# Kernel optimization log

Hardware: AMD Instinct MI355X
Metric: run time of the kernel (lower is better)

The kernel has to match this reference:

```python
import jax, jax.numpy as jnp
import numpy as np

B, T_ENC, T_DEC = 16, 256, 200
N_MELS, ENC_DIM, PRENET, ARNN, DRNN, ATT, NF, KS = 80, 512, 256, 1024, 1024, 128, 32, 31


def _init(k, shape, fan_in):
    return jax.random.normal(k, shape, dtype=jnp.float32) / np.sqrt(fan_in).astype(np.float32)


def setup_inputs() -> dict:
    ks = jax.random.split(jax.random.key(0), 20)
    return {
        "memory": jax.random.normal(ks[0], (B, T_ENC, ENC_DIM), jnp.float32),
        "decoder_inputs": jax.random.normal(ks[1], (B, N_MELS, T_DEC), jnp.float32),
        "memory_lengths": jax.random.randint(ks[2], (B,), T_ENC // 2, T_ENC + 1),
        "prenet_W1": _init(ks[3], (N_MELS, PRENET), N_MELS),
        "prenet_W2": _init(ks[4], (PRENET, PRENET), PRENET),
        "arnn_Wih": _init(ks[5], (PRENET + ENC_DIM, 4 * ARNN), PRENET + ENC_DIM),
        "arnn_Whh": _init(ks[6], (ARNN, 4 * ARNN), ARNN),
        "arnn_b": jnp.zeros((4 * ARNN,), jnp.float32),
        "Wq": _init(ks[7], (ARNN, ATT), ARNN),
        "Wmem": _init(ks[8], (ENC_DIM, ATT), ENC_DIM),
        "v_w": _init(ks[9], (ATT,), ATT),
        "loc_conv_W": _init(ks[10], (NF, 2, KS), 2 * KS),
        "loc_dense_W": _init(ks[11], (NF, ATT), NF),
        "drnn_Wih": _init(ks[12], (ARNN + ENC_DIM, 4 * DRNN), ARNN + ENC_DIM),
        "drnn_Whh": _init(ks[13], (DRNN, 4 * DRNN), DRNN),
        "drnn_b": jnp.zeros((4 * DRNN,), jnp.float32),
        "proj_W": _init(ks[14], (DRNN + ENC_DIM, N_MELS), DRNN + ENC_DIM),
        "proj_b": jnp.zeros((N_MELS,), jnp.float32),
        "gate_W": _init(ks[15], (DRNN + ENC_DIM, 1), DRNN + ENC_DIM),
        "gate_b": jnp.zeros((1,), jnp.float32),
    }


def _lstm_cell(x, h, c, Wih, Whh, b):
    z = x @ Wih + h @ Whh + b  # [B, 4H], torch gate order i,f,g,o
    i, f, g, o = jnp.split(z, 4, axis=-1)
    c_new = jax.nn.sigmoid(f) * c + jax.nn.sigmoid(i) * jnp.tanh(g)
    h_new = jax.nn.sigmoid(o) * jnp.tanh(c_new)
    return h_new, c_new


def reference(memory, decoder_inputs, memory_lengths, prenet_W1, prenet_W2,
              arnn_Wih, arnn_Whh, arnn_b, Wq, Wmem, v_w, loc_conv_W, loc_dense_W,
              drnn_Wih, drnn_Whh, drnn_b, proj_W, proj_b, gate_W, gate_b):
    dt = memory.dtype
    # parse_decoder_inputs + go-frame: [T_DEC+1, B, n_mels]
    di = jnp.transpose(decoder_inputs, (2, 0, 1))
    di = jnp.concatenate([jnp.zeros((1, B, N_MELS), dt), di], axis=0)
    # prenet (dropout hardcoded training=True in source; deterministic key here)
    k1, k2 = jax.random.split(jax.random.key(42))
    x = jax.nn.relu(di @ prenet_W1)
    x = x * jax.random.bernoulli(k1, 0.5, x.shape).astype(dt) * 2.0
    x = jax.nn.relu(x @ prenet_W2)
    x = x * jax.random.bernoulli(k2, 0.5, x.shape).astype(dt) * 2.0
    pre = x[:-1]  # [T_DEC, B, PRENET] (loop consumes first T_DEC frames)

    pm = memory @ Wmem  # processed_memory [B, T_enc, ATT]
    pad_mask = jnp.arange(T_ENC)[None, :] >= memory_lengths[:, None]  # [B, T_enc]
    pad = KS // 2

    def step(carry, xt):
        ah, ac, dh, dc, aw, awc, ctx = carry
        ah, ac = _lstm_cell(jnp.concatenate([xt, ctx], -1), ah, ac, arnn_Wih, arnn_Whh, arnn_b)
        # location-sensitive attention
        awcat = jnp.stack([aw, awc], axis=1)  # [B, 2, T_enc]
        loc = jax.lax.conv_general_dilated(awcat, loc_conv_W, (1,), [(pad, pad)],
                                           dimension_numbers=("NCH", "OIH", "NCH"))  # [B, NF, T_enc]
        loc = jnp.swapaxes(loc, 1, 2) @ loc_dense_W  # [B, T_enc, ATT]
        pq = ah @ Wq  # [B, ATT]
        e = jnp.tanh(pq[:, None, :] + loc + pm) @ v_w  # [B, T_enc]
        e = jnp.where(pad_mask, jnp.asarray(-1e9, dt), e)
        w = jax.nn.softmax(e, axis=1)
        ctx = jnp.einsum("bt,bte->be", w, memory)
        awc = awc + w
        dh, dc = _lstm_cell(jnp.concatenate([ah, ctx], -1), dh, dc, drnn_Wih, drnn_Whh, drnn_b)
        dhc = jnp.concatenate([dh, ctx], axis=1)
        mel = dhc @ proj_W + proj_b  # [B, n_mels]
        gate = (dhc @ gate_W + gate_b)[:, 0]  # [B]
        return (ah, ac, dh, dc, w, awc, ctx), (mel, gate, w)

    carry0 = (jnp.zeros((B, ARNN), dt), jnp.zeros((B, ARNN), dt),
              jnp.zeros((B, DRNN), dt), jnp.zeros((B, DRNN), dt),
              jnp.zeros((B, T_ENC), dt), jnp.zeros((B, T_ENC), dt),
              jnp.zeros((B, ENC_DIM), dt))
    _, (mels, gates, aligns) = jax.lax.scan(step, carry0, pre)
    mel_out = jnp.transpose(mels, (1, 2, 0))    # [B, n_mels, T_DEC]
    gate_out = jnp.transpose(gates, (1, 0))     # [B, T_DEC]
    align_out = jnp.transpose(aligns, (1, 0, 2))  # [B, T_DEC, T_enc]
    return mel_out, gate_out, align_out
```

## Files before the change

kernel.cpp:

```cpp
#include <hip/hip_runtime.h>
#include <stdint.h>

typedef unsigned short u16;
typedef _Float16 h2f16 __attribute__((ext_vector_type(2)));

#define BB    16
#define TENC  256
#define TDEC  200
#define NMELS 80
#define EDIM  512
#define PREN  256
#define ARN   1024
#define ATTN  128
#define NFILT 32
#define KSIZE 31

#define NBLK  256
#define NTHR  1024

#define OFF_AW     0
#define OFF_AWC    4096
#define OFF_AC     8192
#define OFF_DC     24576
#define OFF_XCAT1  40960
#define OFF_XCAT2  77824
#define STATE_F    118784
#define OFF_PRETU  118784
#define OFF_PMU    528384
#define OFF_Z1     790528
#define OFF_Z2     1249280
#define OFF_PQP    1773568
#define OFF_EBUF   1806336
#define OFF_BAR    1810432

__host__ __device__ inline void tf2x32(uint32_t k0, uint32_t k1, uint32_t x0, uint32_t x1,
                                       uint32_t &y0, uint32_t &y1) {
  uint32_t ks2 = k0 ^ k1 ^ 0x1BD11BDAu;
  x0 += k0; x1 += k1;
  const int R0[4] = {13, 15, 26, 6};
  const int R1[4] = {17, 29, 16, 24};
#pragma unroll
  for (int g = 0; g < 5; ++g) {
    const int *R = (g & 1) ? R1 : R0;
#pragma unroll
    for (int i = 0; i < 4; ++i) {
      x0 += x1;
      x1 = (x1 << R[i]) | (x1 >> (32 - R[i]));
      x1 ^= x0;
    }
    switch (g) {
      case 0: x0 += k1;  x1 += ks2 + 1u; break;
      case 1: x0 += ks2; x1 += k0 + 2u;  break;
      case 2: x0 += k0;  x1 += k1 + 3u;  break;
      case 3: x0 += k1;  x1 += ks2 + 4u; break;
      case 4: x0 += ks2; x1 += k0 + 5u;  break;
    }
  }
  y0 = x0; y1 = x1;
}

__device__ inline bool keep_mask(uint32_t k0, uint32_t k1, uint32_t idx) {
  uint32_t y0, y1;
  tf2x32(k0, k1, 0u, idx, y0, y1);
  return (((y0 ^ y1) >> 31) == 0u);
}

__device__ inline float bf2f(u16 v) {
  union { uint32_t u; float f; } x;
  x.u = ((uint32_t)v) << 16;
  return x.f;
}
__device__ inline u16 f2bf(float f) {
  union { float f; uint32_t u; } x;
  x.f = f;
  uint32_t r = ((x.u >> 16) & 1u) + 0x7FFFu;
  return (u16)((x.u + r) >> 16);
}
__device__ inline float sigm(float x) { return 1.f / (1.f + __expf(-x)); }
__device__ inline float ftanh(float x) {
  x = fminf(fmaxf(x, -15.f), 15.f);
  float e = __expf(2.f * x);
  return (e - 1.f) / (e + 1.f);
}

__device__ inline uint32_t packh2(float a, float b) {
  h2f16 h; h[0] = (_Float16)a; h[1] = (_Float16)b;
  union { h2f16 h; uint32_t u; } x; x.h = h; return x.u;
}
__device__ inline h2f16 u2h2(uint32_t u) {
  union { uint32_t u; h2f16 h; } x; x.u = u; return x.h;
}
__device__ inline float fdot2(h2f16 a, h2f16 b, float c) {
#if __has_builtin(__builtin_amdgcn_fdot2)
  return __builtin_amdgcn_fdot2(a, b, c, false);
#else
  return (float)a[0] * (float)b[0] + (float)a[1] * (float)b[1] + c;
#endif
}

__device__ inline float cload(const float *p) {
  uint32_t u = __hip_atomic_load((const uint32_t *)p, __ATOMIC_RELAXED,
                                 __HIP_MEMORY_SCOPE_AGENT);
  union { uint32_t u; float f; } x; x.u = u; return x.f;
}
__device__ inline void cstore(float *p, float v) {
  union { float f; uint32_t u; } x; x.f = v;
  __hip_atomic_store((uint32_t *)p, x.u, __ATOMIC_RELAXED,
                     __HIP_MEMORY_SCOPE_AGENT);
}
__device__ inline void cload8(const float *p, float &a, float &b) {
  unsigned long long u = __hip_atomic_load((const unsigned long long *)p,
                                           __ATOMIC_RELAXED,
                                           __HIP_MEMORY_SCOPE_AGENT);
  union { unsigned long long u; float f[2]; } x; x.u = u;
  a = x.f[0]; b = x.f[1];
}

__device__ inline void gsync(unsigned int *bar, unsigned int e, int cb) {
  __syncthreads();
  if (threadIdx.x == 0) {
    asm volatile("s_waitcnt vmcnt(0)" ::: "memory");
    int g = cb & 7;
    unsigned int *arr = bar + g * 64;
    unsigned int *gct = bar + 512;
    unsigned int *rel = bar + 576 + g * 64;
    unsigned int old = __hip_atomic_fetch_add(arr, 1u, __ATOMIC_RELAXED,
                                              __HIP_MEMORY_SCOPE_AGENT);
    if (old == e * 32u - 1u) {
      unsigned int o2 = __hip_atomic_fetch_add(gct, 1u, __ATOMIC_RELAXED,
                                               __HIP_MEMORY_SCOPE_AGENT);
      if (o2 == e * 8u - 1u) {
#pragma unroll
        for (int g2 = 0; g2 < 8; ++g2)
          __hip_atomic_store(bar + 576 + g2 * 64, e, __ATOMIC_RELAXED,
                             __HIP_MEMORY_SCOPE_AGENT);
      }
    }
    while (__hip_atomic_load(rel, __ATOMIC_RELAXED, __HIP_MEMORY_SCOPE_AGENT) < e)
      __builtin_amdgcn_s_sleep(16);
  }
  __syncthreads();
}

__global__ __launch_bounds__(256) void k_prenet1(const float *__restrict__ dec_in,
                                                 const float *__restrict__ W1,
                                                 u16 *__restrict__ x1,
                                                 uint32_t k0, uint32_t k1) {
  int bid = blockIdx.x;
  int t = bid >> 4, b = bid & 15;
  int tid = threadIdx.x;
  __shared__ float di[NMELS];
  if (tid < NMELS)
    di[tid] = (t == 0) ? 0.f : dec_in[((size_t)b * NMELS + tid) * TDEC + (t - 1)];
  __syncthreads();
  int j = tid;
  float acc = 0.f;
#pragma unroll 4
  for (int m = 0; m < NMELS; ++m) acc += di[m] * W1[(size_t)m * PREN + j];
  acc = fmaxf(acc, 0.f);
  uint32_t idx = ((uint32_t)(t * BB + b)) * PREN + (uint32_t)j;
  acc = keep_mask(k0, k1, idx) ? acc * 2.f : 0.f;
  x1[(t * BB + b) * PREN + j] = f2bf(acc);
}

__global__ __launch_bounds__(256) void k_prenet2(const u16 *__restrict__ x1,
                                                 const float *__restrict__ W2,
                                                 u16 *__restrict__ preTu,
                                                 float *__restrict__ xpre0,
                                                 uint32_t k0, uint32_t k1) {
  int bid = blockIdx.x;
  int t = bid >> 4, b = bid & 15;
  int tid = threadIdx.x;
  __shared__ float xl[PREN];
  xl[tid] = bf2f(x1[(t * BB + b) * PREN + tid]);
  __syncthreads();
  int j = tid;
  float acc = 0.f;
#pragma unroll 4
  for (int k = 0; k < PREN; ++k) acc += xl[k] * W2[(size_t)k * PREN + j];
  acc = fmaxf(acc, 0.f);
  uint32_t idx = ((uint32_t)(t * BB + b)) * PREN + (uint32_t)j;
  acc = keep_mask(k0, k1, idx) ? acc * 2.f : 0.f;
  preTu[(size_t)t * 4096 + j * 16 + b] = f2bf(acc);
  if (t == 0) xpre0[j * 16 + b] = acc;
}

__global__ __launch_bounds__(256) void k_pm(const float *__restrict__ memory,
                                            const float *__restrict__ Wmem,
                                            u16 *__restrict__ pmu) {
  int p = blockIdx.x;
  int b = p & 15, jt = p >> 4;
  int tt = threadIdx.x;
  float acc[32];
#pragma unroll
  for (int j = 0; j < 32; ++j) acc[j] = 0.f;
  const float *mrow = memory + ((size_t)b * TENC + tt) * EDIM;
  const float *wb = Wmem + jt * 32;
  for (int e = 0; e < EDIM; ++e) {
    float mv = mrow[e];
    const float *wr = wb + (size_t)e * ATTN;
#pragma unroll
    for (int j = 0; j < 32; ++j) acc[j] += mv * wr[j];
  }
#pragma unroll
  for (int j = 0; j < 32; ++j)
    pmu[((size_t)(b * ATTN + jt * 32 + j)) * TENC + tt] = f2bf(acc[j]);
}

struct F2 { float x, y; };

union Scr {
  struct { uint32_t xs1[128 * 16]; } z1s;
  struct { uint32_t xs2[160 * 16]; } z2s;
  struct { F2 part[16 * 64]; float hn[64]; } al;
  struct {
    float aw_l[96], awc_l[96];
    float lc[64 * 33];
    float pq[128];
    float ep[64 * 17];
  } att;
  struct { float e_l[256]; float red[32]; float smax, sinv; float part[32 * 33]; } ctc;
  struct { float xl[1536]; float part[12 * 81]; } out;
};

struct KArgs {
  const float *memory; const int *mlen;
  const float *aWih, *aWhh, *ab;
  const float *Wq, *vw, *convW, *ldW;
  const float *dWih, *dWhh, *db;
  const float *projW, *projB, *gateW, *gateB;
  const u16 *preTu, *pmu;
  float *aw, *awc, *ac, *dc, *xcat1, *xcat2, *z1, *z2, *pqp, *ebuf;
  unsigned int *bar;
  float *mel, *gate, *algn;
};

__device__ inline void do_out(const KArgs &A, Scr &s, int b, int tm, int tid) {
  {
    int u = tid;
    float zi = 0.f, zf = 0.f, zg = 0.f, zo = 0.f;
    for (int kc = 0; kc < 8; ++kc) {
      const float *zb = A.z2 + ((size_t)(kc * 16 + b)) * 4096;
      zi += cload(zb + u); zf += cload(zb + u + 1024);
      zg += cload(zb + u + 2048); zo += cload(zb + u + 3072);
    }
    zi += A.db[u]; zf += A.db[u + 1024]; zg += A.db[u + 2048]; zo += A.db[u + 3072];
    float cn = sigm(zf) * A.dc[b * 1024 + u] + sigm(zi) * ftanh(zg);
    float hn = sigm(zo) * ftanh(cn);
    A.dc[b * 1024 + u] = cn;
    cstore(&A.xcat2[(size_t)(1536 + u) * 16 + b], hn);
    s.out.xl[u] = hn;
  }
  if (tid < 512) s.out.xl[1024 + tid] = cload(&A.xcat2[(size_t)(1024 + tid) * 16 + b]);
  __syncthreads();
  if (tid < 960) {
    int col = tid % 80, kc = tid / 80;
    const float *wp = A.projW + (size_t)(kc * 128) * 80 + col;
    const float *xk = s.out.xl + kc * 128;
    float a = 0.f;
#pragma unroll 4
    for (int kk = 0; kk < 128; ++kk) a += xk[kk] * wp[(size_t)kk * 80];
    s.out.part[kc * 81 + col] = a;
  } else if (tid < 972) {
    int kc = tid - 960;
    const float *xk = s.out.xl + kc * 128;
    const float *gk = A.gateW + kc * 128;
    float a = 0.f;
#pragma unroll 4
    for (int kk = 0; kk < 128; ++kk) a += xk[kk] * gk[kk];
    s.out.part[kc * 81 + 80] = a;
  }
  __syncthreads();
  if (tid < 81) {
    float sum = 0.f;
#pragma unroll
    for (int kc = 0; kc < 12; ++kc) sum += s.out.part[kc * 81 + tid];
    if (tid < 80) A.mel[((size_t)b * 80 + tid) * TDEC + tm] = sum + A.projB[tid];
    else          A.gate[(size_t)b * TDEC + tm] = sum + A.gateB[0];
  }
  __syncthreads();
}

__global__ __launch_bounds__(NTHR) void k_persist(KArgs A) {
  __shared__ uint32_t w1h[128 * 128];
  __shared__ uint32_t w2h[160 * 128];
  __shared__ Scr s;
  const int cb = blockIdx.x;
  const int tid = threadIdx.x;
  const int q = cb >> 5;
  const int c = cb & 31;

  if (cb < 224) {
    for (int i = tid; i < 128 * 128; i += NTHR) {
      int k2 = i >> 7, col = i & 127, cg = c * 128 + col;
      int r0 = q * 256 + k2 * 2;
      float f0 = (r0 < 768) ? A.aWih[(size_t)r0 * 4096 + cg]
                            : A.aWhh[(size_t)(r0 - 768) * 4096 + cg];
      float f1 = (r0 < 768) ? A.aWih[(size_t)(r0 + 1) * 4096 + cg]
                            : A.aWhh[(size_t)(r0 - 767) * 4096 + cg];
      w1h[i] = packh2(f0, f1);
    }
  }
  for (int i = tid; i < 160 * 128; i += NTHR) {
    int k2 = i >> 7, col = i & 127, cg = c * 128 + col;
    int r0 = q * 320 + k2 * 2;
    float f0 = (r0 < 1536) ? A.dWih[(size_t)r0 * 4096 + cg]
                           : A.dWhh[(size_t)(r0 - 1536) * 4096 + cg];
    float f1 = (r0 < 1536) ? A.dWih[(size_t)(r0 + 1) * 4096 + cg]
                           : A.dWhh[(size_t)(r0 - 1535) * 4096 + cg];
    w2h[i] = packh2(f0, f1);
  }
  __syncthreads();

  unsigned int ep = 0;
  for (int t = 0; t < TDEC; ++t) {
    const int p = t & 1;

    if (cb < 224) {
      {
        int i = tid;
        int k2 = i >> 3, b2 = (i & 7) * 2;
        int lr = q * 256 + k2 * 2;
        int pr = (lr < 256) ? p * 256 + lr : 256 + lr;
        const float *xr = A.xcat1 + (size_t)pr * 16 + b2;
        float r0a, r0b, r1a, r1b;
        cload8(xr, r0a, r0b);
        cload8(xr + 16, r1a, r1b);
        s.z1s.xs1[k2 * 16 + b2]     = packh2(r0a, r1a);
        s.z1s.xs1[k2 * 16 + b2 + 1] = packh2(r0b, r1b);
      }
      __syncthreads();
      int col = tid & 127, bg = tid >> 7;
      float a0 = 0.f, a1 = 0.f;
      const uint32_t *wp = w1h + col;
      const uint32_t *xp = s.z1s.xs1 + bg * 2;
#pragma unroll 8
      for (int k2 = 0; k2 < 128; ++k2) {
        h2f16 w = u2h2(wp[k2 * 128]);
        a0 = fdot2(w, u2h2(xp[k2 * 16]), a0);
        a1 = fdot2(w, u2h2(xp[k2 * 16 + 1]), a1);
      }
      int cg = c * 128 + col;
      cstore(&A.z1[((size_t)q * 16 + bg * 2    ) * 4096 + cg], a0);
      cstore(&A.z1[((size_t)q * 16 + bg * 2 + 1) * 4096 + cg], a1);
    } else if (cb < 240) {
      if (t > 0) do_out(A, s, cb - 224, t - 1, tid);
    } else if (cb < 242) {
      if (t + 1 < TDEC) {
        int base = ((t + 1) & 1) * 4096;
        int i0 = (cb - 240) * 1024 + tid;
        cstore(&A.xcat1[base + i0],
               bf2f(A.preTu[(size_t)(t + 1) * 4096 + i0]));
        cstore(&A.xcat1[base + i0 + 2048],
               bf2f(A.preTu[(size_t)(t + 1) * 4096 + i0 + 2048]));
      }
    }
    gsync(A.bar, ++ep, cb);

    {
      int b = cb & 15, ug = cb >> 4;
      {
        int u_l = tid & 63, j = tid >> 6;
        int kc = j & 7, gh = j >> 3;
        F2 pv; pv.x = 0.f; pv.y = 0.f;
        if (kc < 7) {
          const float *zb = A.z1 + ((size_t)(kc * 16 + b)) * 4096 + gh * 2048 + (ug * 64 + u_l);
          pv.x = cload(zb); pv.y = cload(zb + 1024);
        }
        s.al.part[j * 64 + u_l] = pv;
      }
      __syncthreads();
      if (tid < 64) {
        int uu = ug * 64 + tid;
        float g0 = 0.f, g1 = 0.f, g2 = 0.f, g3 = 0.f;
#pragma unroll
        for (int kc = 0; kc < 8; ++kc) {
          F2 v0 = s.al.part[kc * 64 + tid];
          F2 v1 = s.al.part[(8 + kc) * 64 + tid];
          g0 += v0.x; g1 += v0.y; g2 += v1.x; g3 += v1.y;
        }
        float zi = g0 + A.ab[uu], zf = g1 + A.ab[1024 + uu];
        float zg = g2 + A.ab[2048 + uu], zo = g3 + A.ab[3072 + uu];
        float cn = sigm(zf) * A.ac[b * 1024 + uu] + sigm(zi) * ftanh(zg);
        float hn = sigm(zo) * ftanh(cn);
        A.ac[b * 1024 + uu] = cn;
        cstore(&A.xcat1[(size_t)(1024 + uu) * 16 + b], hn);
        cstore(&A.xcat2[(size_t)uu * 16 + b], hn);
        s.al.hn[tid] = hn;
      }
      __syncthreads();
      if (tid < 128) {
        float a = 0.f;
        const float *wq = A.Wq + (size_t)(ug * 64) * 128 + tid;
#pragma unroll 4
        for (int k = 0; k < 64; ++k) a += s.al.hn[k] * wq[(size_t)k * 128];
        cstore(&A.pqp[(size_t)(b * 16 + ug) * 128 + tid], a);
      }
    }
    gsync(A.bar, ++ep, cb);

    if (cb < 64) {
      int b = cb & 15, tq = cb >> 4;
      if (tid < 96) {
        int gi = tq * 64 - 16 + tid;
        bool ok = (gi >= 0 && gi < 256);
        s.att.aw_l[tid]  = ok ? cload(&A.aw[b * 256 + gi])  : 0.f;
        s.att.awc_l[tid] = ok ? cload(&A.awc[b * 256 + gi]) : 0.f;
      }
      if (tid >= 128 && tid < 256) {
        int j = tid - 128;
        float sum = 0.f;
#pragma unroll
        for (int g = 0; g < 16; ++g) sum += cload(&A.pqp[(size_t)(b * 16 + g) * 128 + j]);
        s.att.pq[j] = sum;
      }
      __syncthreads();
      {
        int tt_l = tid & 63, fg = tid >> 6;
        int f0 = fg * 2;
        float a0 = 0.f, a1 = 0.f;
        for (int k = 0; k < KSIZE; ++k) {
          float av = s.att.aw_l[tt_l + k + 1];
          float cv = s.att.awc_l[tt_l + k + 1];
          a0 += av * A.convW[f0 * 62 + k]       + cv * A.convW[f0 * 62 + 31 + k];
          a1 += av * A.convW[(f0 + 1) * 62 + k] + cv * A.convW[(f0 + 1) * 62 + 31 + k];
        }
        s.att.lc[tt_l * 33 + f0]     = a0;
        s.att.lc[tt_l * 33 + f0 + 1] = a1;
      }
      __syncthreads();
      {
        int tt_l = tid & 63, g = tid >> 6;
        int tt = tq * 64 + tt_l, j0 = g * 8;
        float acc[8] = {0, 0, 0, 0, 0, 0, 0, 0};
        for (int f = 0; f < NFILT; ++f) {
          float lv = s.att.lc[tt_l * 33 + f];
          const float *lw = A.ldW + f * ATTN + j0;
#pragma unroll
          for (int jj = 0; jj < 8; ++jj) acc[jj] += lv * lw[jj];
        }
        float es = 0.f;
#pragma unroll
        for (int jj = 0; jj < 8; ++jj) {
          float sv = acc[jj] + s.att.pq[j0 + jj]
                   + bf2f(A.pmu[((size_t)(b * 128 + j0 + jj)) * 256 + tt]);
          es += ftanh(sv) * A.vw[j0 + jj];
        }
        s.att.ep[tt_l * 17 + g] = es;
      }
      __syncthreads();
      if (tid < 64) {
        float e = 0.f;
#pragma unroll
        for (int g = 0; g < 16; ++g) e += s.att.ep[tid * 17 + g];
        int tt = tq * 64 + tid;
        if (tt >= A.mlen[b]) e = -1e9f;
        cstore(&A.ebuf[b * 256 + tt], e);
      }
    }
    gsync(A.bar, ++ep, cb);

    {
      int b = cb & 15, ec = cb >> 4;
      if (tid < 256) s.ctc.e_l[tid] = cload(&A.ebuf[b * 256 + tid]);
      __syncthreads();
      if (tid < 32) {
        float m = -1e30f;
#pragma unroll
        for (int i = 0; i < 8; ++i) m = fmaxf(m, s.ctc.e_l[tid * 8 + i]);
        s.ctc.red[tid] = m;
      }
      __syncthreads();
      if (tid == 0) {
        float m = -1e30f;
        for (int i = 0; i < 32; ++i) m = fmaxf(m, s.ctc.red[i]);
        s.ctc.smax = m;
      }
      __syncthreads();
      if (tid < 256) s.ctc.e_l[tid] = __expf(s.ctc.e_l[tid] - s.ctc.smax);
      __syncthreads();
      if (tid < 32) {
        float sm = 0.f;
#pragma unroll
        for (int i = 0; i < 8; ++i) sm += s.ctc.e_l[tid * 8 + i];
        s.ctc.red[tid] = sm;
      }
      __syncthreads();
      if (tid == 0) {
        float sm = 0.f;
        for (int i = 0; i < 32; ++i) sm += s.ctc.red[i];
        s.ctc.sinv = 1.f / sm;
      }
      __syncthreads();
      if (tid < 256) s.ctc.e_l[tid] *= s.ctc.sinv;
      __syncthreads();
      if (ec == 0 && tid < 256) {
        float w = s.ctc.e_l[tid];
        cstore(&A.aw[b * 256 + tid], w);
        cstore(&A.awc[b * 256 + tid], cload(&A.awc[b * 256 + tid]) + w);
        A.algn[((size_t)b * TDEC + t) * TENC + tid] = w;
      }
      {
        int e_l = tid & 31, sub = tid >> 5;
        const float *mp = A.memory + ((size_t)(b * 256) + sub * 8) * 512 + ec * 32 + e_l;
        float a = 0.f;
#pragma unroll
        for (int i = 0; i < 8; ++i) a += s.ctc.e_l[sub * 8 + i] * mp[(size_t)i * 512];
        s.ctc.part[e_l * 33 + sub] = a;
      }
      __syncthreads();
      if (tid < 32) {
        float sum = 0.f;
#pragma unroll
        for (int i = 0; i < 32; ++i) sum += s.ctc.part[tid * 33 + i];
        int eg = ec * 32 + tid;
        cstore(&A.xcat1[(size_t)(512 + eg) * 16 + b], sum);
        cstore(&A.xcat2[(size_t)(1024 + eg) * 16 + b], sum);
      }
    }
    gsync(A.bar, ++ep, cb);

    {
      for (int i = tid; i < 160 * 8; i += NTHR) {
        int k2 = i >> 3, b2 = (i & 7) * 2;
        const float *xr = A.xcat2 + (size_t)(q * 320 + k2 * 2) * 16 + b2;
        float r0a, r0b, r1a, r1b;
        cload8(xr, r0a, r0b);
        cload8(xr + 16, r1a, r1b);
        s.z2s.xs2[k2 * 16 + b2]     = packh2(r0a, r1a);
        s.z2s.xs2[k2 * 16 + b2 + 1] = packh2(r0b, r1b);
      }
      __syncthreads();
      int col = tid & 127, bg = tid >> 7;
      float a0 = 0.f, a1 = 0.f;
      const uint32_t *wp = w2h + col;
      const uint32_t *xp = s.z2s.xs2 + bg * 2;
#pragma unroll 8
      for (int k2 = 0; k2 < 160; ++k2) {
        h2f16 w = u2h2(wp[k2 * 128]);
        a0 = fdot2(w, u2h2(xp[k2 * 16]), a0);
        a1 = fdot2(w, u2h2(xp[k2 * 16 + 1]), a1);
      }
      int cg = c * 128 + col;
      cstore(&A.z2[((size_t)q * 16 + bg * 2    ) * 4096 + cg], a0);
      cstore(&A.z2[((size_t)q * 16 + bg * 2 + 1) * 4096 + cg], a1);
    }
    gsync(A.bar, ++ep, cb);
  }

  if (cb >= 224 && cb < 240) do_out(A, s, cb - 224, TDEC - 1, tid);
}

extern "C" void kernel_launch(void *const *d_in, const int *in_sizes, int n_in,
                              void *d_out, int out_size, void *d_ws, size_t ws_size,
                              hipStream_t stream) {
  (void)in_sizes; (void)n_in; (void)out_size; (void)ws_size;
  const float *memory = (const float *)d_in[0];
  const float *dec_in = (const float *)d_in[1];
  const int   *mlen   = (const int *)d_in[2];
  const float *pw1    = (const float *)d_in[3];
  const float *pw2    = (const float *)d_in[4];
  const float *aWih   = (const float *)d_in[5];
  const float *aWhh   = (const float *)d_in[6];
  const float *ab     = (const float *)d_in[7];
  const float *wq     = (const float *)d_in[8];
  const float *wmem   = (const float *)d_in[9];
  const float *vw     = (const float *)d_in[10];
  const float *convW  = (const float *)d_in[11];
  const float *ldW    = (const float *)d_in[12];
  const float *dWih   = (const float *)d_in[13];
  const float *dWhh   = (const float *)d_in[14];
  const float *db     = (const float *)d_in[15];
  const float *projW  = (const float *)d_in[16];
  const float *projB  = (const float *)d_in[17];
  const float *gateW  = (const float *)d_in[18];
  const float *gateB  = (const float *)d_in[19];

  float *out_mel  = (float *)d_out;
  float *out_gate = out_mel + (size_t)16 * 80 * 200;
  float *out_algn = out_gate + (size_t)16 * 200;

  float *ws = (float *)d_ws;
  float *aw    = ws + OFF_AW;
  float *awc   = ws + OFF_AWC;
  float *ac    = ws + OFF_AC;
  float *dc    = ws + OFF_DC;
  float *xcat1 = ws + OFF_XCAT1;
  float *xcat2 = ws + OFF_XCAT2;
  u16 *preTu = (u16 *)(ws + OFF_PRETU);
  u16 *pmu   = (u16 *)(ws + OFF_PMU);
  float *z1   = ws + OFF_Z1;
  float *z2   = ws + OFF_Z2;
  float *pqp  = ws + OFF_PQP;
  float *ebuf = ws + OFF_EBUF;
  unsigned int *bar = (unsigned int *)(ws + OFF_BAR);
  u16 *x1u   = (u16 *)z1;

  hipMemsetAsync(ws, 0, STATE_F * sizeof(float), stream);
  hipMemsetAsync(bar, 0, 2048 * sizeof(unsigned int), stream);

  uint32_t K1a, K1b, K2a, K2b;
  tf2x32(0u, 42u, 0u, 0u, K1a, K1b);
  tf2x32(0u, 42u, 0u, 1u, K2a, K2b);

  k_prenet1<<<TDEC * BB, 256, 0, stream>>>(dec_in, pw1, x1u, K1a, K1b);
  k_prenet2<<<TDEC * BB, 256, 0, stream>>>(x1u, pw2, preTu, xcat1, K2a, K2b);
  k_pm<<<64, 256, 0, stream>>>(memory, wmem, pmu);

  KArgs ka;
  ka.memory = memory; ka.mlen = mlen;
  ka.aWih = aWih; ka.aWhh = aWhh; ka.ab = ab;
  ka.Wq = wq; ka.vw = vw; ka.convW = convW; ka.ldW = ldW;
  ka.dWih = dWih; ka.dWhh = dWhh; ka.db = db;
  ka.projW = projW; ka.projB = projB; ka.gateW = gateW; ka.gateB = gateB;
  ka.preTu = preTu; ka.pmu = pmu;
  ka.aw = aw; ka.awc = awc; ka.ac = ac; ka.dc = dc;
  ka.xcat1 = xcat1; ka.xcat2 = xcat2; ka.z1 = z1; ka.z2 = z2;
  ka.pqp = pqp; ka.ebuf = ebuf;
  ka.bar = bar;
  ka.mel = out_mel; ka.gate = out_gate; ka.algn = out_algn;

  void *kp[] = { &ka };
  hipLaunchCooperativeKernel((void *)k_persist, dim3(NBLK), dim3(NTHR), kp, 0, stream);
}
```

Measured before the change: 25.44 ms.

## Store recurrent LSTM input vectors pre-packed as fp16 pairs in global memory

```diff
diff --git a/kernel.cpp b/kernel.cpp
--- a/kernel.cpp
+++ b/kernel.cpp
@@ -22,16 +22,17 @@
 #define OFF_AWC    4096
 #define OFF_AC     8192
 #define OFF_DC     24576
-#define OFF_XCAT1  40960
-#define OFF_XCAT2  77824
-#define STATE_F    118784
-#define OFF_PRETU  118784
-#define OFF_PMU    528384
-#define OFF_Z1     790528
-#define OFF_Z2     1249280
-#define OFF_PQP    1773568
-#define OFF_EBUF   1806336
-#define OFF_BAR    1810432
+#define OFF_X1P    40960
+#define OFF_X2P    57344
+#define OFF_CTXF   77824
+#define STATE_F    86016
+#define OFF_PRETU  86016
+#define OFF_PMU    495616
+#define OFF_Z1     757760
+#define OFF_Z2     1216512
+#define OFF_PQP    1740800
+#define OFF_EBUF   1773568
+#define OFF_BAR    1777664
 
 __host__ __device__ inline void tf2x32(uint32_t k0, uint32_t k1, uint32_t x0, uint32_t x1,
                                        uint32_t &y0, uint32_t &y1) {
@@ -108,12 +109,11 @@
   __hip_atomic_store((uint32_t *)p, x.u, __ATOMIC_RELAXED,
                      __HIP_MEMORY_SCOPE_AGENT);
 }
-__device__ inline void cload8(const float *p, float &a, float &b) {
-  unsigned long long u = __hip_atomic_load((const unsigned long long *)p,
-                                           __ATOMIC_RELAXED,
-                                           __HIP_MEMORY_SCOPE_AGENT);
-  union { unsigned long long u; float f[2]; } x; x.u = u;
-  a = x.f[0]; b = x.f[1];
+__device__ inline uint32_t cload_u32(const uint32_t *p) {
+  return __hip_atomic_load(p, __ATOMIC_RELAXED, __HIP_MEMORY_SCOPE_AGENT);
+}
+__device__ inline void cstore_u32(uint32_t *p, uint32_t v) {
+  __hip_atomic_store(p, v, __ATOMIC_RELAXED, __HIP_MEMORY_SCOPE_AGENT);
 }
 
 __device__ inline void gsync(unsigned int *bar, unsigned int e, int cb) {
@@ -165,8 +165,8 @@
 
 __global__ __launch_bounds__(256) void k_prenet2(const u16 *__restrict__ x1,
                                                  const float *__restrict__ W2,
-                                                 u16 *__restrict__ preTu,
-                                                 float *__restrict__ xpre0,
+                                                 uint32_t *__restrict__ preTuP,
+                                                 uint32_t *__restrict__ x1p,
                                                  uint32_t k0, uint32_t k1) {
   int bid = blockIdx.x;
   int t = bid >> 4, b = bid & 15;
@@ -181,8 +181,12 @@
   acc = fmaxf(acc, 0.f);
   uint32_t idx = ((uint32_t)(t * BB + b)) * PREN + (uint32_t)j;
   acc = keep_mask(k0, k1, idx) ? acc * 2.f : 0.f;
-  preTu[(size_t)t * 4096 + j * 16 + b] = f2bf(acc);
-  if (t == 0) xpre0[j * 16 + b] = acc;
+  float accN = __shfl_down(acc, 1);
+  if (!(j & 1)) {
+    uint32_t pk = packh2(acc, accN);
+    preTuP[(size_t)t * 2048 + (j >> 1) * 16 + b] = pk;
+    if (t == 0) x1p[(j >> 1) * 16 + b] = pk;
+  }
 }
 
 __global__ __launch_bounds__(256) void k_pm(const float *__restrict__ memory,
@@ -229,8 +233,9 @@
   const float *Wq, *vw, *convW, *ldW;
   const float *dWih, *dWhh, *db;
   const float *projW, *projB, *gateW, *gateB;
-  const u16 *preTu, *pmu;
-  float *aw, *awc, *ac, *dc, *xcat1, *xcat2, *z1, *z2, *pqp, *ebuf;
+  const uint32_t *preTuP; const u16 *pmu;
+  uint32_t *x1p, *x2p;
+  float *aw, *awc, *ac, *dc, *ctxf, *z1, *z2, *pqp, *ebuf;
   unsigned int *bar;
   float *mel, *gate, *algn;
 };
@@ -248,10 +253,12 @@
     float cn = sigm(zf) * A.dc[b * 1024 + u] + sigm(zi) * ftanh(zg);
     float hn = sigm(zo) * ftanh(cn);
     A.dc[b * 1024 + u] = cn;
-    cstore(&A.xcat2[(size_t)(1536 + u) * 16 + b], hn);
+    float hn2 = __shfl_down(hn, 1);
+    if (!(tid & 1))
+      cstore_u32(A.x2p + (size_t)(768 + (tid >> 1)) * 16 + b, packh2(hn, hn2));
     s.out.xl[u] = hn;
   }
-  if (tid < 512) s.out.xl[1024 + tid] = cload(&A.xcat2[(size_t)(1024 + tid) * 16 + b]);
+  if (tid < 512) s.out.xl[1024 + tid] = cload(A.ctxf + (size_t)tid * 16 + b);
   __syncthreads();
   if (tid < 960) {
     int col = tid % 80, kc = tid / 80;
@@ -317,17 +324,13 @@
     const int p = t & 1;
 
     if (cb < 224) {
-      {
-        int i = tid;
-        int k2 = i >> 3, b2 = (i & 7) * 2;
-        int lr = q * 256 + k2 * 2;
-        int pr = (lr < 256) ? p * 256 + lr : 256 + lr;
-        const float *xr = A.xcat1 + (size_t)pr * 16 + b2;
-        float r0a, r0b, r1a, r1b;
-        cload8(xr, r0a, r0b);
-        cload8(xr + 16, r1a, r1b);
-        s.z1s.xs1[k2 * 16 + b2]     = packh2(r0a, r1a);
-        s.z1s.xs1[k2 * 16 + b2 + 1] = packh2(r0b, r1b);
+#pragma unroll
+      for (int rep = 0; rep < 2; ++rep) {
+        int i = tid + rep * 1024;
+        int k2 = i >> 4, b = i & 15;
+        int lp = q * 128 + k2;
+        int pp = (lp < 128) ? p * 128 + lp : 128 + lp;
+        s.z1s.xs1[i] = cload_u32(A.x1p + (size_t)pp * 16 + b);
       }
       __syncthreads();
       int col = tid & 127, bg = tid >> 7;
@@ -347,12 +350,9 @@
       if (t > 0) do_out(A, s, cb - 224, t - 1, tid);
     } else if (cb < 242) {
       if (t + 1 < TDEC) {
-        int base = ((t + 1) & 1) * 4096;
-        int i0 = (cb - 240) * 1024 + tid;
-        cstore(&A.xcat1[base + i0],
-               bf2f(A.preTu[(size_t)(t + 1) * 4096 + i0]));
-        cstore(&A.xcat1[base + i0 + 2048],
-               bf2f(A.preTu[(size_t)(t + 1) * 4096 + i0 + 2048]));
+        int i = (cb - 240) * 1024 + tid;
+        cstore_u32(A.x1p + (size_t)(((t + 1) & 1) * 128) * 16 + i,
+                   cload_u32(A.preTuP + (size_t)(t + 1) * 2048 + i));
       }
     }
     gsync(A.bar, ++ep, cb);
@@ -384,9 +384,14 @@
         float cn = sigm(zf) * A.ac[b * 1024 + uu] + sigm(zi) * ftanh(zg);
         float hn = sigm(zo) * ftanh(cn);
         A.ac[b * 1024 + uu] = cn;
-        cstore(&A.xcat1[(size_t)(1024 + uu) * 16 + b], hn);
-        cstore(&A.xcat2[(size_t)uu * 16 + b], hn);
         s.al.hn[tid] = hn;
+        float hn2 = __shfl_down(hn, 1);
+        if (!(tid & 1)) {
+          uint32_t pk = packh2(hn, hn2);
+          int prw = uu >> 1;
+          cstore_u32(A.x1p + (size_t)(512 + prw) * 16 + b, pk);
+          cstore_u32(A.x2p + (size_t)prw * 16 + b, pk);
+        }
       }
       __syncthreads();
       if (tid < 128) {
@@ -514,21 +519,22 @@
 #pragma unroll
         for (int i = 0; i < 32; ++i) sum += s.ctc.part[tid * 33 + i];
         int eg = ec * 32 + tid;
-        cstore(&A.xcat1[(size_t)(512 + eg) * 16 + b], sum);
-        cstore(&A.xcat2[(size_t)(1024 + eg) * 16 + b], sum);
+        cstore(&A.ctxf[(size_t)eg * 16 + b], sum);
+        float s2 = __shfl_down(sum, 1);
+        if (!(tid & 1)) {
+          uint32_t pk = packh2(sum, s2);
+          int prw = eg >> 1;
+          cstore_u32(A.x1p + (size_t)(256 + prw) * 16 + b, pk);
+          cstore_u32(A.x2p + (size_t)(512 + prw) * 16 + b, pk);
+        }
       }
     }
     gsync(A.bar, ++ep, cb);
 
     {
-      for (int i = tid; i < 160 * 8; i += NTHR) {
-        int k2 = i >> 3, b2 = (i & 7) * 2;
-        const float *xr = A.xcat2 + (size_t)(q * 320 + k2 * 2) * 16 + b2;
-        float r0a, r0b, r1a, r1b;
-        cload8(xr, r0a, r0b);
-        cload8(xr + 16, r1a, r1b);
-        s.z2s.xs2[k2 * 16 + b2]     = packh2(r0a, r1a);
-        s.z2s.xs2[k2 * 16 + b2 + 1] = packh2(r0b, r1b);
+      for (int i = tid; i < 160 * 16; i += NTHR) {
+        int k2 = i >> 4, b = i & 15;
+        s.z2s.xs2[i] = cload_u32(A.x2p + (size_t)(q * 160 + k2) * 16 + b);
       }
       __syncthreads();
       int col = tid & 127, bg = tid >> 7;
@@ -585,9 +591,10 @@
   float *awc   = ws + OFF_AWC;
   float *ac    = ws + OFF_AC;
   float *dc    = ws + OFF_DC;
-  float *xcat1 = ws + OFF_XCAT1;
-  float *xcat2 = ws + OFF_XCAT2;
-  u16 *preTu = (u16 *)(ws + OFF_PRETU);
+  uint32_t *x1p = (uint32_t *)(ws + OFF_X1P);
+  uint32_t *x2p = (uint32_t *)(ws + OFF_X2P);
+  float *ctxf  = ws + OFF_CTXF;
+  uint32_t *preTuP = (uint32_t *)(ws + OFF_PRETU);
   u16 *pmu   = (u16 *)(ws + OFF_PMU);
   float *z1   = ws + OFF_Z1;
   float *z2   = ws + OFF_Z2;
@@ -604,7 +611,7 @@
   tf2x32(0u, 42u, 0u, 1u, K2a, K2b);
 
   k_prenet1<<<TDEC * BB, 256, 0, stream>>>(dec_in, pw1, x1u, K1a, K1b);
-  k_prenet2<<<TDEC * BB, 256, 0, stream>>>(x1u, pw2, preTu, xcat1, K2a, K2b);
+  k_prenet2<<<TDEC * BB, 256, 0, stream>>>(x1u, pw2, preTuP, x1p, K2a, K2b);
   k_pm<<<64, 256, 0, stream>>>(memory, wmem, pmu);
 
   KArgs ka;
@@ -613,10 +620,10 @@
   ka.Wq = wq; ka.vw = vw; ka.convW = convW; ka.ldW = ldW;
   ka.dWih = dWih; ka.dWhh = dWhh; ka.db = db;
   ka.projW = projW; ka.projB = projB; ka.gateW = gateW; ka.gateB = gateB;
-  ka.preTu = preTu; ka.pmu = pmu;
-  ka.aw = aw; ka.awc = awc; ka.ac = ac; ka.dc = dc;
-  ka.xcat1 = xcat1; ka.xcat2 = xcat2; ka.z1 = z1; ka.z2 = z2;
-  ka.pqp = pqp; ka.ebuf = ebuf;
+  ka.preTuP = preTuP; ka.pmu = pmu;
+  ka.x1p = x1p; ka.x2p = x2p;
+  ka.aw = aw; ka.awc = awc; ka.ac = ac; ka.dc = dc; ka.ctxf = ctxf;
+  ka.z1 = z1; ka.z2 = z2; ka.pqp = pqp; ka.ebuf = ebuf;
   ka.bar = bar;
   ka.mel = out_mel; ka.gate = out_gate; ka.algn = out_algn;
 
```

New measurement: 25.39 ms. Within noise of the previous version (-0.2%).
